# Kernel tuning notes

Measured on AMD Instinct MI355X. Metric: run time of the kernel, lower is better.

Reference implementation:

```python
import jax, jax.numpy as jnp
import numpy as np
import math

N_HEADS = 16
EMBED = 1024
D_KEY = EMBED // N_HEADS
B, S = 2, 2048
NEG = -1000000000.0


def setup_inputs() -> dict:
    key = jax.random.key(0)
    ks = jax.random.split(key, 7)
    scale = 1.0 / math.sqrt(EMBED)
    x = jax.random.normal(ks[0], (B, S, EMBED), dtype=jnp.float32)
    Wq_w = jax.random.uniform(ks[1], (EMBED, EMBED), jnp.float32, -scale, scale)
    Wq_b = jax.random.uniform(ks[2], (EMBED,), jnp.float32, -scale, scale)
    Wk_w = jax.random.uniform(ks[3], (EMBED, EMBED), jnp.float32, -scale, scale)
    Wk_b = jax.random.uniform(ks[4], (EMBED,), jnp.float32, -scale, scale)
    Wv_w = jax.random.uniform(ks[5], (EMBED, EMBED), jnp.float32, -scale, scale)
    Wv_b = jax.random.uniform(ks[6], (EMBED,), jnp.float32, -scale, scale)
    return {"x": x, "Wq_w": Wq_w, "Wq_b": Wq_b, "Wk_w": Wk_w, "Wk_b": Wk_b,
            "Wv_w": Wv_w, "Wv_b": Wv_b, "is_masked": 1}


def reference(x, Wq_w, Wq_b, Wk_w, Wk_b, Wv_w, Wv_b, is_masked):
    b, s, e = x.shape
    # nn.Linear: y = x @ W.T + b
    q = x @ Wq_w.T + Wq_b
    k = x @ Wk_w.T + Wk_b
    v = x @ Wv_w.T + Wv_b
    # [B, H, S, Dk]
    q = q.reshape(b, s, N_HEADS, D_KEY).transpose(0, 2, 1, 3)
    k = k.reshape(b, s, N_HEADS, D_KEY).transpose(0, 2, 1, 3)
    v = v.reshape(b, s, N_HEADS, D_KEY).transpose(0, 2, 1, 3)
    scores = jnp.einsum("bhqd,bhkd->bhqk", q, k) / math.sqrt(D_KEY)
    # non-standard mask: keep positions where score != padding (0)
    mask = scores != 0.0
    if is_masked:
        causal = jnp.tril(jnp.ones((1, s, s), dtype=bool))  # broadcasts over B,H
        mask = causal[None] & mask  # [1,1,S,S] & [B,H,S,S]
    scores = jnp.where(mask, scores, NEG)
    probs = jax.nn.softmax(scores, axis=-1)
    out = jnp.einsum("bhqk,bhkd->bhqd", probs, v)
    return out.transpose(0, 2, 1, 3).reshape(b, s, e)
```

## Files before the change

### kernel.cpp

```cpp
#include <hip/hip_runtime.h>

#define B_SZ   2
#define NH     16
#define S_LEN  2048
#define DK     64
#define EMB    1024
#define M_TOT  (B_SZ * S_LEN)
#define KT     64

typedef float          f32x4  __attribute__((ext_vector_type(4)));
typedef float          f32x16 __attribute__((ext_vector_type(16)));
typedef unsigned int   u32x4  __attribute__((ext_vector_type(4)));
typedef unsigned short u16x8  __attribute__((ext_vector_type(8)));
typedef unsigned short u16x4  __attribute__((ext_vector_type(4)));
typedef __bf16         bf16x8 __attribute__((ext_vector_type(8)));

static __device__ __forceinline__ f32x4 mfma16(u16x8 a, u16x8 b, f32x4 c) {
    return __builtin_amdgcn_mfma_f32_16x16x32_bf16(
        __builtin_bit_cast(bf16x8, a), __builtin_bit_cast(bf16x8, b), c, 0, 0, 0);
}
static __device__ __forceinline__ f32x16 mfma32(u16x8 a, u16x8 b, f32x16 c) {
    return __builtin_amdgcn_mfma_f32_32x32x16_bf16(
        __builtin_bit_cast(bf16x8, a), __builtin_bit_cast(bf16x8, b), c, 0, 0, 0);
}

static __device__ __forceinline__ unsigned short f2bf(float f) {
    unsigned int u = __builtin_bit_cast(unsigned int, f);
    u = (u + 0x7FFFu + ((u >> 16) & 1u)) >> 16;
    return (unsigned short)u;
}

static __device__ __forceinline__ float exp2_hw(float x) {
    float r; asm("v_exp_f32 %0, %1" : "=v"(r) : "v"(x)); return r;
}

static __device__ __forceinline__ void barrier_raw() {
    asm volatile("s_barrier" ::: "memory");
}
#define VMCNT8() asm volatile("s_waitcnt vmcnt(8)" ::: "memory")
#define VMCNT4() asm volatile("s_waitcnt vmcnt(4)" ::: "memory")
#define VMCNT0() asm volatile("s_waitcnt vmcnt(0)" ::: "memory")

#define GLDS16(g, l)  __builtin_amdgcn_global_load_lds(                      \
    (const void __attribute__((address_space(1)))*)(g),                      \
    (void __attribute__((address_space(3)))*)(l), 16, 0, 0)

__global__ __launch_bounds__(256) void cvt_kernel(
    const float* __restrict__ x,  const float* __restrict__ wq,
    const float* __restrict__ wk, const float* __restrict__ wv,
    unsigned short* __restrict__ xb,  unsigned short* __restrict__ wqb,
    unsigned short* __restrict__ wkb, unsigned short* __restrict__ wvb)
{
    long gid = (long)blockIdx.x * 256 + threadIdx.x;
    long e = gid * 4;
    const float* src; unsigned short* dst; long off;
    if      (e < 4194304L) { src = x;  dst = xb;  off = e; }
    else if (e < 5242880L) { src = wq; dst = wqb; off = e - 4194304L; }
    else if (e < 6291456L) { src = wk; dst = wkb; off = e - 5242880L; }
    else                   { src = wv; dst = wvb; off = e - 6291456L; }
    f32x4 v = *(const f32x4*)(src + off);
    u16x4 u;
    u[0] = f2bf(v[0]); u[1] = f2bf(v[1]); u[2] = f2bf(v[2]); u[3] = f2bf(v[3]);
    *(u16x4*)(dst + off) = u;
}

__global__ __launch_bounds__(512) void qkv_gemm(
    const unsigned short* __restrict__ xb,
    const unsigned short* __restrict__ wb,
    const float* __restrict__ bq, const float* __restrict__ bk,
    const float* __restrict__ bv,
    unsigned short* __restrict__ qkv)
{
    const int tid  = threadIdx.x;
    const int lane = tid & 63;
    const int wid  = tid >> 6;
    const int wm   = wid >> 2, wn = wid & 3;
    const int lid  = blockIdx.y * 12 + blockIdx.x;
    const int nid  = (lid & 7) * 24 + (lid >> 3);
    const int n0   = (nid >> 4) * 256;
    const int m0   = (nid & 15) * 256;
    const int l15  = lane & 15;
    const int k4   = lane >> 4;

    __shared__ __align__(16) unsigned short Al[4][256 * 32];
    __shared__ __align__(16) unsigned short Bl[4][256 * 32];

    f32x4 acc[8][4];
#pragma unroll
    for (int i = 0; i < 8; ++i)
#pragma unroll
        for (int j = 0; j < 4; ++j)
            acc[i][j] = (f32x4){0.f, 0.f, 0.f, 0.f};

    const int row0 = tid >> 2, row1 = (512 + tid) >> 2;
    const int sl   = tid & 3;
    const int c0   = (sl ^ (row0 & 3)) << 3;
    const int c1   = (sl ^ (row1 & 3)) << 3;
    const int d0   = (wid * 64) * 8;
    const int d1   = (512 + wid * 64) * 8;
    const unsigned short* gA0 = xb + (size_t)(m0 + row0) * EMB + c0;
    const unsigned short* gA1 = xb + (size_t)(m0 + row1) * EMB + c1;
    const unsigned short* gB0 = wb + (size_t)(n0 + row0) * EMB + c0;
    const unsigned short* gB1 = wb + (size_t)(n0 + row1) * EMB + c1;

#define STAGE_A(kt, b) do {                                     \
        GLDS16(gA0 + (kt) * 32, &Al[b][d0]);                    \
        GLDS16(gA1 + (kt) * 32, &Al[b][d1]); } while (0)
#define STAGE_B(kt, b) do {                                     \
        GLDS16(gB0 + (kt) * 32, &Bl[b][d0]);                    \
        GLDS16(gB1 + (kt) * 32, &Bl[b][d1]); } while (0)

    const int rsl = (k4 ^ (l15 & 3)) << 3;
    const int abase = wm * 128 + l15;
    const int bbase = wn * 64 + l15;

    STAGE_A(0, 0); STAGE_B(0, 0);
    STAGE_A(1, 1); STAGE_B(1, 1);
    STAGE_A(2, 2); STAGE_B(2, 2);
    VMCNT8();
    barrier_raw();

    for (int kt = 0; kt < 32; ++kt) {
        const int b = kt & 3;
        const unsigned short* Ab = Al[b];
        const unsigned short* Bb = Bl[b];

        u16x8 bfr[4], afr[4];
#pragma unroll
        for (int j = 0; j < 4; ++j)
            bfr[j] = *(const u16x8*)&Bb[(bbase + j * 16) * 32 + rsl];
#pragma unroll
        for (int i = 0; i < 4; ++i)
            afr[i] = *(const u16x8*)&Ab[(abase + i * 16) * 32 + rsl];
        if (kt + 3 < 32) STAGE_A(kt + 3, (kt + 3) & 3);
        __builtin_amdgcn_s_setprio(1);
#pragma unroll
        for (int i = 0; i < 4; ++i)
#pragma unroll
            for (int j = 0; j < 4; ++j)
                acc[i][j] = mfma16(afr[i], bfr[j], acc[i][j]);
        __builtin_amdgcn_s_setprio(0);
        barrier_raw();

#pragma unroll
        for (int i = 0; i < 4; ++i)
            afr[i] = *(const u16x8*)&Ab[(abase + (4 + i) * 16) * 32 + rsl];
        if (kt + 3 < 32) STAGE_B(kt + 3, (kt + 3) & 3);
        __builtin_amdgcn_s_setprio(1);
#pragma unroll
        for (int i = 0; i < 4; ++i)
#pragma unroll
            for (int j = 0; j < 4; ++j)
                acc[4 + i][j] = mfma16(afr[i], bfr[j], acc[4 + i][j]);
        __builtin_amdgcn_s_setprio(0);

        if (kt == 29)      VMCNT4();
        else if (kt == 30) VMCNT0();
        else               VMCNT8();
        barrier_raw();
    }

    const int mat = n0 >> 10;
    const float* bias = (mat == 0) ? bq : ((mat == 1) ? bk : bv);
    unsigned short* dst = qkv + (size_t)mat * ((size_t)M_TOT * EMB);
    const int nb = (n0 & 1023) + wn * 64;
#pragma unroll
    for (int fc = 0; fc < 4; ++fc) {
        const int nl = nb + fc * 16 + l15;
        const float bvv = bias[nl];
        const int h = nl >> 6, d = nl & 63;
#pragma unroll
        for (int fr = 0; fr < 8; ++fr) {
#pragma unroll
            for (int rr = 0; rr < 4; ++rr) {
                const int m = m0 + wm * 128 + fr * 16 + k4 * 4 + rr;
                const int bb = m >> 11, s = m & 2047;
                dst[((size_t)((bb * NH + h) * S_LEN + s)) * DK + d] =
                    f2bf(acc[fr][fc][rr] + bvv);
            }
        }
    }
#undef STAGE_A
#undef STAGE_B
}

__global__ __launch_bounds__(512) void attn_kernel(
    const unsigned short* __restrict__ Q,
    const unsigned short* __restrict__ K,
    const unsigned short* __restrict__ V,
    const int* __restrict__ mskp,
    float* __restrict__ out)
{
    const int tid = threadIdx.x, lane = tid & 63, wid = tid >> 6;
    const int grp = wid >> 2, qw = wid & 3;
    const int l31 = lane & 31, H = lane >> 5;
    const int bh = blockIdx.x;
    const int h  = bh & 15, b = bh >> 4;
    const int yp = blockIdx.y;
    const size_t hoff = ((size_t)(b * NH + h)) * S_LEN * DK;
    const unsigned short* Qh = Q + hoff;
    const unsigned short* Kh = K + hoff;
    const unsigned short* Vh = V + hoff;
    const int msk = *mskp;

    __shared__ __align__(16) unsigned short Kl[2][2][64 * 64];
    __shared__ __align__(16) unsigned short Vt[2][2][64 * 64];
    __shared__ float MLbuf[512];

    u16x8 ones1;
#pragma unroll
    for (int i = 0; i < 8; ++i) ones1[i] = 0x3F80;

    const int gt  = tid & 255;
    const int sr0 = gt >> 3, sc8 = gt & 7, sr1 = sr0 + 32;
    const int kwo0 = sr0 * 64 + ((sc8 ^ (sr0 & 7)) << 3);
    const int kwo1 = sr1 * 64 + ((sc8 ^ (sr1 & 7)) << 3);
    const int vwo0 = (((sr0 >> 3) ^ sc8) << 3) + (sr0 & 7);
    const int vwo1 = (((sr1 >> 3) ^ sc8) << 3) + (sr1 & 7);

    const int dsw0 = l31 >> 3, dsw1 = 4 + (l31 >> 3);
    const int rsw  = l31 & 7;
    const float SC2 = 0.125f * 1.4426950408889634f;
    const int idx  = qw * 64 + lane;

    for (int seg = 0; seg < 2; ++seg) {
        const int qt = seg ? (15 - yp) : yp;
        const int q0 = qt * 128;
        const int ntiles = msk ? (2 * qt + 2) : (S_LEN / KT);
        const int niter  = ntiles >> 1;
        const int qrow = q0 + qw * 32 + l31;
        const int qmin = q0 + qw * 32;

        u16x8 qf[4];
#pragma unroll
        for (int ks = 0; ks < 4; ++ks)
            qf[ks] = *(const u16x8*)(Qh + (size_t)qrow * DK + ks * 16 + H * 8);

        f32x16 o0, o1, lacc;
#pragma unroll
        for (int i = 0; i < 16; ++i) { o0[i] = 0.f; o1[i] = 0.f; lacc[i] = 0.f; }
        float mx = -1e30f;

        u16x8 kr[2], vr[2];
        {
            const unsigned short* K0 = Kh + (size_t)grp * KT * DK;
            const unsigned short* V0 = Vh + (size_t)grp * KT * DK;
            kr[0] = *(const u16x8*)(K0 + (size_t)sr0 * DK + sc8 * 8);
            vr[0] = *(const u16x8*)(V0 + (size_t)sr0 * DK + sc8 * 8);
            kr[1] = *(const u16x8*)(K0 + (size_t)sr1 * DK + sc8 * 8);
            vr[1] = *(const u16x8*)(V0 + (size_t)sr1 * DK + sc8 * 8);
        }
        __syncthreads();
        {
            unsigned short* Kg = Kl[grp][0];
            unsigned short* Vg = Vt[grp][0];
            *(u16x8*)&Kg[kwo0] = kr[0];
            *(u16x8*)&Kg[kwo1] = kr[1];
#pragma unroll
            for (int e = 0; e < 8; ++e) {
                Vg[(sc8 * 8 + e) * 64 + vwo0] = vr[0][e];
                Vg[(sc8 * 8 + e) * 64 + vwo1] = vr[1][e];
            }
            if (grp + 2 < ntiles) {
                const unsigned short* Kn = Kh + (size_t)(grp + 2) * KT * DK;
                const unsigned short* Vn = Vh + (size_t)(grp + 2) * KT * DK;
                kr[0] = *(const u16x8*)(Kn + (size_t)sr0 * DK + sc8 * 8);
                vr[0] = *(const u16x8*)(Vn + (size_t)sr0 * DK + sc8 * 8);
                kr[1] = *(const u16x8*)(Kn + (size_t)sr1 * DK + sc8 * 8);
                vr[1] = *(const u16x8*)(Vn + (size_t)sr1 * DK + sc8 * 8);
            }
        }
        __syncthreads();

        int cur = 0;
        for (int it = 0; it < niter; ++it) {
            const int kt = 2 * it + grp;

            if (kt + 2 < ntiles) {
                unsigned short* Kg = Kl[grp][cur ^ 1];
                unsigned short* Vg = Vt[grp][cur ^ 1];
                *(u16x8*)&Kg[kwo0] = kr[0];
                *(u16x8*)&Kg[kwo1] = kr[1];
#pragma unroll
                for (int e = 0; e < 8; ++e) {
                    Vg[(sc8 * 8 + e) * 64 + vwo0] = vr[0][e];
                    Vg[(sc8 * 8 + e) * 64 + vwo1] = vr[1][e];
                }
            }
            if (kt + 4 < ntiles) {
                const unsigned short* Kn = Kh + (size_t)(kt + 4) * KT * DK;
                const unsigned short* Vn = Vh + (size_t)(kt + 4) * KT * DK;
                kr[0] = *(const u16x8*)(Kn + (size_t)sr0 * DK + sc8 * 8);
                vr[0] = *(const u16x8*)(Vn + (size_t)sr0 * DK + sc8 * 8);
                kr[1] = *(const u16x8*)(Kn + (size_t)sr1 * DK + sc8 * 8);
                vr[1] = *(const u16x8*)(Vn + (size_t)sr1 * DK + sc8 * 8);
            }

            if (!(msk && kt * KT > qmin + 31)) {
                const unsigned short* Kg = Kl[grp][cur];
                const unsigned short* Vg = Vt[grp][cur];

                f32x16 st0, st1;
#pragma unroll
                for (int i = 0; i < 16; ++i) { st0[i] = 0.f; st1[i] = 0.f; }
#pragma unroll
                for (int ks = 0; ks < 4; ++ks) {
                    const int g = (((ks << 1) + H) ^ rsw) << 3;
                    u16x8 kf0 = *(const u16x8*)&Kg[l31 * 64 + g];
                    u16x8 kf1 = *(const u16x8*)&Kg[(32 + l31) * 64 + g];
                    st0 = mfma32(kf0, qf[ks], st0);
                    st1 = mfma32(kf1, qf[ks], st1);
                }

                st0 *= SC2;
                st1 *= SC2;
                float p[32];
#pragma unroll
                for (int r = 0; r < 16; ++r) { p[r] = st0[r]; p[16 + r] = st1[r]; }
                const bool needmask = msk && (kt * KT + 63 > qrow);
                if (needmask) {
#pragma unroll
                    for (int r = 0; r < 16; ++r) {
                        const int krow = (r & 3) + 8 * (r >> 2) + 4 * H;
                        if (kt * KT + krow > qrow)      p[r]      = -1e30f;
                        if (kt * KT + 32 + krow > qrow) p[16 + r] = -1e30f;
                    }
                }

                float t8[8];
#pragma unroll
                for (int i = 0; i < 8; ++i)
                    t8[i] = fmaxf(fmaxf(p[i], p[i + 8]), fmaxf(p[i + 16], p[i + 24]));
#pragma unroll
                for (int i = 0; i < 4; ++i) t8[i] = fmaxf(t8[i], t8[i + 4]);
                float mt = fmaxf(fmaxf(t8[0], t8[1]), fmaxf(t8[2], t8[3]));
                mt = fmaxf(mt, __shfl_xor(mt, 32, 64));

                if (!__all(mt <= mx + 11.54f)) {
                    const float mn = fmaxf(mx, mt);
                    const float al = exp2_hw(mx - mn);
                    mx = mn;
                    o0 *= al; o1 *= al;
                    lacc[0] *= al;
                }

#pragma unroll
                for (int r = 0; r < 32; ++r) p[r] = exp2_hw(p[r] - mx);

#pragma unroll
                for (int ks = 0; ks < 4; ++ks) {
                    const int bb = ks * 8;
                    unsigned int wa, wb2, wc, wd;
                    asm("v_cvt_pk_bf16_f32 %0, %1, %2" : "=v"(wa)  : "v"(p[bb + 0]), "v"(p[bb + 1]));
                    asm("v_cvt_pk_bf16_f32 %0, %1, %2" : "=v"(wb2) : "v"(p[bb + 2]), "v"(p[bb + 3]));
                    asm("v_cvt_pk_bf16_f32 %0, %1, %2" : "=v"(wc)  : "v"(p[bb + 4]), "v"(p[bb + 5]));
                    asm("v_cvt_pk_bf16_f32 %0, %1, %2" : "=v"(wd)  : "v"(p[bb + 6]), "v"(p[bb + 7]));
                    asm volatile("v_permlane32_swap_b32 %0, %1" : "+v"(wa),  "+v"(wc));
                    asm volatile("v_permlane32_swap_b32 %0, %1" : "+v"(wb2), "+v"(wd));
                    u32x4 wv; wv[0] = wa; wv[1] = wb2; wv[2] = wc; wv[3] = wd;
                    const u16x8 pb = __builtin_bit_cast(u16x8, wv);
                    const int kg = (ks << 1) + H;
                    u16x8 vf0 = *(const u16x8*)&Vg[l31 * 64        + ((kg ^ dsw0) << 3)];
                    u16x8 vf1 = *(const u16x8*)&Vg[(32 + l31) * 64 + ((kg ^ dsw1) << 3)];
                    o0 = mfma32(vf0, pb, o0);
                    o1 = mfma32(vf1, pb, o1);
                    lacc = mfma32(ones1, pb, lacc);
                }
            }

            __syncthreads();
            cur ^= 1;
        }

        float* MO = (float*)Kl + idx * 32;
        const float lsum = lacc[0];
        if (grp == 1) {
#pragma unroll
            for (int i = 0; i < 16; ++i) {
                MO[(i + idx) & 31]      = o0[i];
                MO[(16 + i + idx) & 31] = o1[i];
            }
            MLbuf[idx * 2]     = mx;
            MLbuf[idx * 2 + 1] = lsum;
        }
        __syncthreads();
        if (grp == 0) {
            const float m2 = MLbuf[idx * 2], l2 = MLbuf[idx * 2 + 1];
            const float mn = fmaxf(mx, m2);
            const float ea = exp2_hw(mx - mn);
            const float eb = exp2_hw(m2 - mn);
            const float inv = 1.f / (lsum * ea + l2 * eb);
            float* orow = out + ((size_t)(b * S_LEN) + qrow) * EMB + h * DK;
#pragma unroll
            for (int g = 0; g < 4; ++g) {
                f32x4 w0, w1;
#pragma unroll
                for (int i = 0; i < 4; ++i) {
                    w0[i] = (o0[4 * g + i] * ea + MO[(4 * g + i + idx) & 31] * eb) * inv;
                    w1[i] = (o1[4 * g + i] * ea + MO[(16 + 4 * g + i + idx) & 31] * eb) * inv;
                }
                *(f32x4*)&orow[8 * g + 4 * H]      = w0;
                *(f32x4*)&orow[32 + 8 * g + 4 * H] = w1;
            }
        }
    }
}

extern "C" void kernel_launch(void* const* d_in, const int* in_sizes, int n_in,
                              void* d_out, int out_size, void* d_ws, size_t ws_size,
                              hipStream_t stream)
{
    const float* x  = (const float*)d_in[0];
    const float* wq = (const float*)d_in[1];
    const float* bq = (const float*)d_in[2];
    const float* wk = (const float*)d_in[3];
    const float* bk = (const float*)d_in[4];
    const float* wv = (const float*)d_in[5];
    const float* bv = (const float*)d_in[6];
    const int* msk  = (const int*)d_in[7];
    float* out = (float*)d_out;

    unsigned short* xb  = (unsigned short*)d_ws;
    unsigned short* wb  = xb + (size_t)M_TOT * EMB;
    unsigned short* qkv = wb + (size_t)3 * 1024 * 1024;

    cvt_kernel<<<7168, 256, 0, stream>>>(x, wq, wk, wv,
                                         xb, wb, wb + 1024 * 1024, wb + 2 * 1024 * 1024);
    qkv_gemm<<<dim3(12, 16, 1), 512, 0, stream>>>(xb, wb, bq, bk, bv, qkv);
    attn_kernel<<<dim3(32, 8, 1), 512, 0, stream>>>(
        qkv, qkv + (size_t)M_TOT * EMB, qkv + (size_t)2 * M_TOT * EMB, msk, out);
}
```

Before: 86.01 us.

## Shrink QKV GEMM tiles to 128x128 and split attention MFMA accumulator chains

The QKV GEMM moves from 256x256 tiles with 512 threads and a 4-stage A/B-split pipeline to 128x128 tiles with 256 threads, a 3-stage ring buffer and one combined staging step per k-iteration. The grid grows from 192 to 768 blocks, which should fill the CUs better, at the cost of lower per-block data reuse and more global traffic. Separately, the attention kernel splits its QK^T and PV MFMA accumulators into two independent chains summed at the end. This shortens dependent MFMA chains but raises accumulator register pressure.

```diff
diff --git a/kernel.cpp b/kernel.cpp
--- a/kernel.cpp
+++ b/kernel.cpp
@@ -37,7 +37,6 @@
 static __device__ __forceinline__ void barrier_raw() {
     asm volatile("s_barrier" ::: "memory");
 }
-#define VMCNT8() asm volatile("s_waitcnt vmcnt(8)" ::: "memory")
 #define VMCNT4() asm volatile("s_waitcnt vmcnt(4)" ::: "memory")
 #define VMCNT0() asm volatile("s_waitcnt vmcnt(0)" ::: "memory")
 
@@ -64,7 +63,7 @@
     *(u16x4*)(dst + off) = u;
 }
 
-__global__ __launch_bounds__(512) void qkv_gemm(
+__global__ __launch_bounds__(256) void qkv_gemm(
     const unsigned short* __restrict__ xb,
     const unsigned short* __restrict__ wb,
     const float* __restrict__ bq, const float* __restrict__ bk,
@@ -74,90 +73,78 @@
     const int tid  = threadIdx.x;
     const int lane = tid & 63;
     const int wid  = tid >> 6;
-    const int wm   = wid >> 2, wn = wid & 3;
-    const int lid  = blockIdx.y * 12 + blockIdx.x;
-    const int nid  = (lid & 7) * 24 + (lid >> 3);
-    const int n0   = (nid >> 4) * 256;
-    const int m0   = (nid & 15) * 256;
+    const int wm   = wid >> 1, wn = wid & 1;
+    const int lid  = blockIdx.y * 24 + blockIdx.x;
+    const int nid  = (lid & 7) * 96 + (lid >> 3);
+    const int n0   = (nid >> 5) * 128;
+    const int m0   = (nid & 31) * 128;
     const int l15  = lane & 15;
     const int k4   = lane >> 4;
 
-    __shared__ __align__(16) unsigned short Al[4][256 * 32];
-    __shared__ __align__(16) unsigned short Bl[4][256 * 32];
-
-    f32x4 acc[8][4];
-#pragma unroll
-    for (int i = 0; i < 8; ++i)
+    __shared__ __align__(16) unsigned short Al[3][128 * 32];
+    __shared__ __align__(16) unsigned short Bl[3][128 * 32];
+
+    f32x4 acc[4][4];
+#pragma unroll
+    for (int i = 0; i < 4; ++i)
 #pragma unroll
         for (int j = 0; j < 4; ++j)
             acc[i][j] = (f32x4){0.f, 0.f, 0.f, 0.f};
 
-    const int row0 = tid >> 2, row1 = (512 + tid) >> 2;
+    const int row0 = tid >> 2, row1 = 64 + row0;
     const int sl   = tid & 3;
     const int c0   = (sl ^ (row0 & 3)) << 3;
     const int c1   = (sl ^ (row1 & 3)) << 3;
     const int d0   = (wid * 64) * 8;
-    const int d1   = (512 + wid * 64) * 8;
+    const int d1   = (256 + wid * 64) * 8;
     const unsigned short* gA0 = xb + (size_t)(m0 + row0) * EMB + c0;
     const unsigned short* gA1 = xb + (size_t)(m0 + row1) * EMB + c1;
     const unsigned short* gB0 = wb + (size_t)(n0 + row0) * EMB + c0;
     const unsigned short* gB1 = wb + (size_t)(n0 + row1) * EMB + c1;
 
-#define STAGE_A(kt, b) do {                                     \
+#define STAGE(kt, b) do {                                       \
         GLDS16(gA0 + (kt) * 32, &Al[b][d0]);                    \
-        GLDS16(gA1 + (kt) * 32, &Al[b][d1]); } while (0)
-#define STAGE_B(kt, b) do {                                     \
+        GLDS16(gA1 + (kt) * 32, &Al[b][d1]);                    \
         GLDS16(gB0 + (kt) * 32, &Bl[b][d0]);                    \
         GLDS16(gB1 + (kt) * 32, &Bl[b][d1]); } while (0)
 
     const int rsl = (k4 ^ (l15 & 3)) << 3;
-    const int abase = wm * 128 + l15;
+    const int abase = wm * 64 + l15;
     const int bbase = wn * 64 + l15;
 
-    STAGE_A(0, 0); STAGE_B(0, 0);
-    STAGE_A(1, 1); STAGE_B(1, 1);
-    STAGE_A(2, 2); STAGE_B(2, 2);
-    VMCNT8();
+    STAGE(0, 0);
+    STAGE(1, 1);
+    VMCNT4();
     barrier_raw();
 
+    int bufsel = 0;
     for (int kt = 0; kt < 32; ++kt) {
-        const int b = kt & 3;
-        const unsigned short* Ab = Al[b];
-        const unsigned short* Bb = Bl[b];
-
-        u16x8 bfr[4], afr[4];
+        const unsigned short* Ab = Al[bufsel];
+        const unsigned short* Bb = Bl[bufsel];
+
+        u16x8 a[4], b4[4];
+#pragma unroll
+        for (int i = 0; i < 4; ++i)
+            a[i] = *(const u16x8*)&Ab[(abase + i * 16) * 32 + rsl];
 #pragma unroll
         for (int j = 0; j < 4; ++j)
-            bfr[j] = *(const u16x8*)&Bb[(bbase + j * 16) * 32 + rsl];
+            b4[j] = *(const u16x8*)&Bb[(bbase + j * 16) * 32 + rsl];
+
+        int nb3 = bufsel + 2; if (nb3 >= 3) nb3 -= 3;
+        if (kt + 2 < 32) STAGE(kt + 2, nb3);
+
+        __builtin_amdgcn_s_setprio(1);
 #pragma unroll
         for (int i = 0; i < 4; ++i)
-            afr[i] = *(const u16x8*)&Ab[(abase + i * 16) * 32 + rsl];
-        if (kt + 3 < 32) STAGE_A(kt + 3, (kt + 3) & 3);
-        __builtin_amdgcn_s_setprio(1);
-#pragma unroll
-        for (int i = 0; i < 4; ++i)
 #pragma unroll
             for (int j = 0; j < 4; ++j)
-                acc[i][j] = mfma16(afr[i], bfr[j], acc[i][j]);
+                acc[i][j] = mfma16(a[i], b4[j], acc[i][j]);
         __builtin_amdgcn_s_setprio(0);
+
+        if (kt == 30) VMCNT0(); else VMCNT4();
         barrier_raw();
 
-#pragma unroll
-        for (int i = 0; i < 4; ++i)
-            afr[i] = *(const u16x8*)&Ab[(abase + (4 + i) * 16) * 32 + rsl];
-        if (kt + 3 < 32) STAGE_B(kt + 3, (kt + 3) & 3);
-        __builtin_amdgcn_s_setprio(1);
-#pragma unroll
-        for (int i = 0; i < 4; ++i)
-#pragma unroll
-            for (int j = 0; j < 4; ++j)
-                acc[4 + i][j] = mfma16(afr[i], bfr[j], acc[4 + i][j]);
-        __builtin_amdgcn_s_setprio(0);
-
-        if (kt == 29)      VMCNT4();
-        else if (kt == 30) VMCNT0();
-        else               VMCNT8();
-        barrier_raw();
+        bufsel += 1; if (bufsel >= 3) bufsel -= 3;
     }
 
     const int mat = n0 >> 10;
@@ -170,18 +157,17 @@
         const float bvv = bias[nl];
         const int h = nl >> 6, d = nl & 63;
 #pragma unroll
-        for (int fr = 0; fr < 8; ++fr) {
+        for (int fr = 0; fr < 4; ++fr) {
 #pragma unroll
             for (int rr = 0; rr < 4; ++rr) {
-                const int m = m0 + wm * 128 + fr * 16 + k4 * 4 + rr;
+                const int m = m0 + wm * 64 + fr * 16 + k4 * 4 + rr;
                 const int bb = m >> 11, s = m & 2047;
                 dst[((size_t)((bb * NH + h) * S_LEN + s)) * DK + d] =
                     f2bf(acc[fr][fc][rr] + bvv);
             }
         }
     }
-#undef STAGE_A
-#undef STAGE_B
+#undef STAGE
 }
 
 __global__ __launch_bounds__(512) void attn_kernel(
@@ -236,9 +222,12 @@
         for (int ks = 0; ks < 4; ++ks)
             qf[ks] = *(const u16x8*)(Qh + (size_t)qrow * DK + ks * 16 + H * 8);
 
-        f32x16 o0, o1, lacc;
-#pragma unroll
-        for (int i = 0; i < 16; ++i) { o0[i] = 0.f; o1[i] = 0.f; lacc[i] = 0.f; }
+        f32x16 o0a, o0b, o1a, o1b, lacc;
+#pragma unroll
+        for (int i = 0; i < 16; ++i) {
+            o0a[i] = 0.f; o0b[i] = 0.f; o1a[i] = 0.f; o1b[i] = 0.f;
+            lacc[i] = 0.f;
+        }
         float mx = -1e30f;
 
         u16x8 kr[2], vr[2];
@@ -300,20 +289,30 @@
                 const unsigned short* Kg = Kl[grp][cur];
                 const unsigned short* Vg = Vt[grp][cur];
 
-                f32x16 st0, st1;
-#pragma unroll
-                for (int i = 0; i < 16; ++i) { st0[i] = 0.f; st1[i] = 0.f; }
-#pragma unroll
-                for (int ks = 0; ks < 4; ++ks) {
+                f32x16 st0a, st0b, st1a, st1b;
+#pragma unroll
+                for (int i = 0; i < 16; ++i) {
+                    st0a[i] = 0.f; st0b[i] = 0.f; st1a[i] = 0.f; st1b[i] = 0.f;
+                }
+#pragma unroll
+                for (int ks = 0; ks < 2; ++ks) {
                     const int g = (((ks << 1) + H) ^ rsw) << 3;
                     u16x8 kf0 = *(const u16x8*)&Kg[l31 * 64 + g];
                     u16x8 kf1 = *(const u16x8*)&Kg[(32 + l31) * 64 + g];
-                    st0 = mfma32(kf0, qf[ks], st0);
-                    st1 = mfma32(kf1, qf[ks], st1);
-                }
-
-                st0 *= SC2;
-                st1 *= SC2;
+                    st0a = mfma32(kf0, qf[ks], st0a);
+                    st1a = mfma32(kf1, qf[ks], st1a);
+                }
+#pragma unroll
+                for (int ks = 2; ks < 4; ++ks) {
+                    const int g = (((ks << 1) + H) ^ rsw) << 3;
+                    u16x8 kf0 = *(const u16x8*)&Kg[l31 * 64 + g];
+                    u16x8 kf1 = *(const u16x8*)&Kg[(32 + l31) * 64 + g];
+                    st0b = mfma32(kf0, qf[ks], st0b);
+                    st1b = mfma32(kf1, qf[ks], st1b);
+                }
+                f32x16 st0 = (st0a + st0b) * SC2;
+                f32x16 st1 = (st1a + st1b) * SC2;
+
                 float p[32];
 #pragma unroll
                 for (int r = 0; r < 16; ++r) { p[r] = st0[r]; p[16 + r] = st1[r]; }
@@ -340,7 +339,7 @@
                     const float mn = fmaxf(mx, mt);
                     const float al = exp2_hw(mx - mn);
                     mx = mn;
-                    o0 *= al; o1 *= al;
+                    o0a *= al; o0b *= al; o1a *= al; o1b *= al;
                     lacc[0] *= al;
                 }
 
@@ -362,8 +361,13 @@
                     const int kg = (ks << 1) + H;
                     u16x8 vf0 = *(const u16x8*)&Vg[l31 * 64        + ((kg ^ dsw0) << 3)];
                     u16x8 vf1 = *(const u16x8*)&Vg[(32 + l31) * 64 + ((kg ^ dsw1) << 3)];
-                    o0 = mfma32(vf0, pb, o0);
-                    o1 = mfma32(vf1, pb, o1);
+                    if (ks < 2) {
+                        o0a = mfma32(vf0, pb, o0a);
+                        o1a = mfma32(vf1, pb, o1a);
+                    } else {
+                        o0b = mfma32(vf0, pb, o0b);
+                        o1b = mfma32(vf1, pb, o1b);
+                    }
                     lacc = mfma32(ones1, pb, lacc);
                 }
             }
@@ -371,6 +375,9 @@
             __syncthreads();
             cur ^= 1;
         }
+
+        const f32x16 o0 = o0a + o0b;
+        const f32x16 o1 = o1a + o1b;
 
         float* MO = (float*)Kl + idx * 32;
         const float lsum = lacc[0];
@@ -426,7 +433,7 @@
 
     cvt_kernel<<<7168, 256, 0, stream>>>(x, wq, wk, wv,
                                          xb, wb, wb + 1024 * 1024, wb + 2 * 1024 * 1024);
-    qkv_gemm<<<dim3(12, 16, 1), 512, 0, stream>>>(xb, wb, bq, bk, bv, qkv);
+    qkv_gemm<<<dim3(24, 32, 1), 256, 0, stream>>>(xb, wb, bq, bk, bv, qkv);
     attn_kernel<<<dim3(32, 8, 1), 512, 0, stream>>>(
         qkv, qkv + (size_t)M_TOT * EMB, qkv + (size_t)2 * M_TOT * EMB, msk, out);
 }
```

Result: slower. 105.5 us (+22.7%).
